# Kernel tuning notes

Measured on AMD Instinct MI355X. Metric: run time of the kernel, lower is better.

Reference implementation:

```python
import jax, jax.numpy as jnp
import numpy as np


def setup_inputs() -> dict:
    key = jax.random.key(0)
    k1, k2, k3 = jax.random.split(key, 3)
    B, S, D, O, C = 4, 1024, 1024, 1024, 8
    x = jax.random.normal(k1, (B, S, D), dtype=jnp.float32)
    category_id = jax.random.randint(k2, (B, S), 0, C, dtype=jnp.int64)
    weight = jax.random.normal(k3, (C, D, O), dtype=jnp.float32)
    bias = jnp.zeros((C, O), dtype=jnp.float32)
    return {"x": x, "category_id": category_id, "weight": weight, "bias": bias}


def reference(x, category_id, weight, bias):
    # Faithful to: out[t] = x[t] @ weight[cid[t]] + bias[cid[t]]
    # Instead of gathering a full [T, D, O] per-token weight tensor (the torch
    # original's bmm formulation), compute x against every category's matrix and
    # select the row for each token's category -- same math, far less memory.
    orig_shape = x.shape
    T = np.prod(orig_shape[:-1])
    x_flat = x.reshape(T, orig_shape[-1])            # [T, D]
    cid = category_id.reshape(T)                      # [T]
    y_all = jnp.einsum('td,cdo->tco', x_flat, weight)  # [T, C, O]
    y = jnp.take_along_axis(y_all, cid[:, None, None], axis=1)[:, 0, :]  # [T, O]
    out = y + bias[cid]                               # [T, O]
    return out.reshape(*orig_shape[:-1], out.shape[-1])
```

## Files before the change

kernel.cpp:

```cpp
#include <hip/hip_runtime.h>


typedef __attribute__((ext_vector_type(8))) short bf16x8;
typedef __attribute__((ext_vector_type(4))) float f32x4;
typedef __attribute__((ext_vector_type(8))) unsigned short ushort8_t;

__device__ __forceinline__ unsigned short f2bf(float f) {
  unsigned u = __float_as_uint(f);
  u += 0x7FFFu + ((u >> 16) & 1u);
  return (unsigned short)(u >> 16);
}

__device__ __forceinline__ void gload_lds16(const unsigned short* g, unsigned short* l) {
  __builtin_amdgcn_global_load_lds(
      (const __attribute__((address_space(1))) unsigned int*)g,
      (__attribute__((address_space(3))) unsigned int*)l, 16, 0, 0);
}

#define MAXC 8

__global__ void k_prep(const float* __restrict__ W, unsigned short* __restrict__ Wt,
                       int Dd, int Oo,
                       const float* __restrict__ x, unsigned short* __restrict__ xb, int nX,
                       const int* __restrict__ cid, int* __restrict__ counts,
                       int* __restrict__ bucket, int T, int C, int tpw) {
  int b   = blockIdx.x;
  int tid = threadIdx.x;

  if (b == 0) {
    __shared__ int cnt[256][MAXC];
    int tpt = (T + 255) / 256;
    int t0  = tid * tpt;
    int t1  = min(t0 + tpt, T);
    for (int c = 0; c < C; ++c) cnt[tid][c] = 0;
    for (int t = t0; t < t1; ++t) cnt[tid][cid[t]]++;
    __syncthreads();
    if (tid < C) {
      int run = 0;
      for (int t = 0; t < 256; ++t) { int v = cnt[t][tid]; cnt[t][tid] = run; run += v; }
      counts[tid] = run;
    }
    __syncthreads();
    for (int t = t0; t < t1; ++t) {
      int c = cid[t];
      int p = cnt[tid][c]++;
      bucket[c * T + p] = t;
    }
    return;
  }

  if (b > tpw) {
    int i = ((b - tpw - 1) * 256 + tid) * 8;
    if (i >= nX) return;
    float4 a0 = *reinterpret_cast<const float4*>(x + i);
    float4 a1 = *reinterpret_cast<const float4*>(x + i + 4);
    ushort8_t o;
    o[0] = f2bf(a0.x); o[1] = f2bf(a0.y); o[2] = f2bf(a0.z); o[3] = f2bf(a0.w);
    o[4] = f2bf(a1.x); o[5] = f2bf(a1.y); o[6] = f2bf(a1.z); o[7] = f2bf(a1.w);
    *reinterpret_cast<ushort8_t*>(xb + i) = o;
    return;
  }

  int bb  = b - 1;
  int tpc = (Dd / 64) * (Oo / 64);
  int c   = bb / tpc;
  int rem = bb % tpc;
  int d0  = (rem / (Oo / 64)) * 64;
  int o0  = (rem % (Oo / 64)) * 64;

  __shared__ float t[64][65];
  const float* Wc = W + (size_t)c * Dd * Oo;
#pragma unroll
  for (int p = 0; p < 4; ++p) {
    int chunk = p * 256 + tid;
    int r  = chunk >> 4;
    int cb = chunk & 15;
    float4 v = *reinterpret_cast<const float4*>(Wc + (size_t)(d0 + r) * Oo + o0 + cb * 4);
    t[r][cb * 4 + 0] = v.x; t[r][cb * 4 + 1] = v.y;
    t[r][cb * 4 + 2] = v.z; t[r][cb * 4 + 3] = v.w;
  }
  __syncthreads();
  unsigned short* Wtc = Wt + (size_t)c * Oo * Dd;
#pragma unroll
  for (int p = 0; p < 2; ++p) {
    int chunk = p * 256 + tid;
    int orow = chunk >> 3;
    int dseg = chunk & 7;
    ushort8_t w;
#pragma unroll
    for (int j = 0; j < 8; ++j) w[j] = f2bf(t[dseg * 8 + j][orow]);
    *reinterpret_cast<ushort8_t*>(Wtc + (size_t)(o0 + orow) * Dd + d0 + dseg * 8) = w;
  }
}

#define BM 128
#define BN 128
#define BK 64
#define TILE_A (BM * BK)
#define TILE_B (BN * BK)

__global__ __launch_bounds__(1024) void k_ggemm(
    const unsigned short* __restrict__ xb, const unsigned short* __restrict__ Wt,
    const float* __restrict__ bias, const int* __restrict__ counts,
    const int* __restrict__ bucket, float* __restrict__ out,
    int T, int Dd, int Oo) {
  int c  = blockIdx.x;
  int Mc = counts[c];
  int m0 = blockIdx.z * BM;
  if (m0 >= Mc) return;
  int n0 = blockIdx.y * BN;

  extern __shared__ __align__(16) unsigned short smem[];
  unsigned short* Al = smem;
  unsigned short* Bl = smem + 3 * TILE_A;

  const int tid  = threadIdx.x;
  const int lane = tid & 63;
  const int wid  = tid >> 6;
  const int wm   = wid >> 2, wn = wid & 3;

  const int* buck = bucket + c * T;
  const unsigned short* Wc = Wt + (size_t)c * Oo * Dd;

  const unsigned short* aSrc;
  const unsigned short* bSrc;
  int sOff;
  {
    int row = wid * 8 + (lane >> 3);
    int seg = (lane & 7) ^ (row & 7);
    int mr  = m0 + row;
    int tok = buck[mr < Mc ? mr : Mc - 1];
    aSrc = xb + (size_t)tok * Dd + seg * 8;
    bSrc = Wc + (size_t)(n0 + row) * Dd + seg * 8;
    sOff = (wid * 8) * BK;
  }

  float bias_r[2];
#pragma unroll
  for (int ni = 0; ni < 2; ++ni)
    bias_r[ni] = bias[c * Oo + n0 + wn * 32 + ni * 16 + (lane & 15)];

  const f32x4 fzero = {0.f, 0.f, 0.f, 0.f};
  f32x4 acc[2][2];
#pragma unroll
  for (int i = 0; i < 2; ++i)
#pragma unroll
    for (int j = 0; j < 2; ++j) acc[i][j] = fzero;

  const int KT = Dd / BK;

#pragma unroll
  for (int t8 = 0; t8 < 2; ++t8) {
    int ko = t8 * BK;
    gload_lds16(aSrc + ko, Al + t8 * TILE_A + sOff);
    gload_lds16(bSrc + ko, Bl + t8 * TILE_B + sOff);
  }

  for (int kt = 0; kt < KT; ++kt) {
    int cur = kt % 3;
    asm volatile("s_waitcnt lgkmcnt(0)" ::: "memory");
    if (kt < KT - 1) {
      asm volatile("s_waitcnt vmcnt(2)" ::: "memory");
    } else {
      asm volatile("s_waitcnt vmcnt(0)" ::: "memory");
    }
    __builtin_amdgcn_sched_barrier(0);
    __builtin_amdgcn_s_barrier();
    __builtin_amdgcn_sched_barrier(0);

    int nb = (cur + 2 >= 3) ? cur - 1 : cur + 2;
    if (kt + 2 < KT) gload_lds16(aSrc + (kt + 2) * BK, Al + nb * TILE_A + sOff);
    {
      bf16x8 af[2], bf[2];
#pragma unroll
      for (int mi = 0; mi < 2; ++mi) {
        int row  = wm * 32 + mi * 16 + (lane & 15);
        int slot = (lane >> 4) ^ (row & 7);
        af[mi] = *reinterpret_cast<const bf16x8*>(&Al[cur * TILE_A + row * BK + slot * 8]);
      }
#pragma unroll
      for (int ni = 0; ni < 2; ++ni) {
        int row  = wn * 32 + ni * 16 + (lane & 15);
        int slot = (lane >> 4) ^ (row & 7);
        bf[ni] = *reinterpret_cast<const bf16x8*>(&Bl[cur * TILE_B + row * BK + slot * 8]);
      }
      __builtin_amdgcn_s_setprio(1);
#pragma unroll
      for (int mi = 0; mi < 2; ++mi)
#pragma unroll
        for (int ni = 0; ni < 2; ++ni)
          acc[mi][ni] = __builtin_amdgcn_mfma_f32_16x16x32_bf16(af[mi], bf[ni], acc[mi][ni], 0, 0, 0);
      __builtin_amdgcn_s_setprio(0);
    }
    __builtin_amdgcn_sched_barrier(0);
    __builtin_amdgcn_s_barrier();
    __builtin_amdgcn_sched_barrier(0);
    if (kt + 2 < KT) gload_lds16(bSrc + (kt + 2) * BK, Bl + nb * TILE_B + sOff);
    {
      bf16x8 af[2], bf[2];
#pragma unroll
      for (int mi = 0; mi < 2; ++mi) {
        int row  = wm * 32 + mi * 16 + (lane & 15);
        int slot = (4 + (lane >> 4)) ^ (row & 7);
        af[mi] = *reinterpret_cast<const bf16x8*>(&Al[cur * TILE_A + row * BK + slot * 8]);
      }
#pragma unroll
      for (int ni = 0; ni < 2; ++ni) {
        int row  = wn * 32 + ni * 16 + (lane & 15);
        int slot = (4 + (lane >> 4)) ^ (row & 7);
        bf[ni] = *reinterpret_cast<const bf16x8*>(&Bl[cur * TILE_B + row * BK + slot * 8]);
      }
      __builtin_amdgcn_s_setprio(1);
#pragma unroll
      for (int mi = 0; mi < 2; ++mi)
#pragma unroll
        for (int ni = 0; ni < 2; ++ni)
          acc[mi][ni] = __builtin_amdgcn_mfma_f32_16x16x32_bf16(af[mi], bf[ni], acc[mi][ni], 0, 0, 0);
      __builtin_amdgcn_s_setprio(0);
    }
  }

#pragma unroll
  for (int mi = 0; mi < 2; ++mi) {
    int rb = m0 + wm * 32 + mi * 16 + (lane >> 4) * 4;
#pragma unroll
    for (int r = 0; r < 4; ++r) {
      int mrow = rb + r;
      if (mrow < Mc) {
        int tok = buck[mrow];
        float* orow = out + (size_t)tok * Oo;
#pragma unroll
        for (int ni = 0; ni < 2; ++ni) {
          int col = n0 + wn * 32 + ni * 16 + (lane & 15);
          orow[col] = acc[mi][ni][r] + bias_r[ni];
        }
      }
    }
  }
}

extern "C" void kernel_launch(void* const* d_in, const int* in_sizes, int n_in,
                              void* d_out, int out_size, void* d_ws, size_t ws_size,
                              hipStream_t stream) {
  const float* x    = (const float*)d_in[0];
  const int*   cid  = (const int*)d_in[1];
  const float* W    = (const float*)d_in[2];
  const float* bias = (const float*)d_in[3];
  float* out = (float*)d_out;

  int T = in_sizes[1];
  int D = in_sizes[0] / T;
  int O = out_size / T;
  int C = in_sizes[3] / O;

  char* ws = (char*)d_ws;
  int* counts = (int*)ws;
  int* bucket = (int*)(ws + 64);
  unsigned short* xb = (unsigned short*)(ws + 64 + (size_t)C * T * 4);
  unsigned short* Wt = xb + (size_t)T * D;

  int tpw  = C * (D / 64) * (O / 64);
  int cvtb = (T * D / 8 + 255) / 256;
  k_prep<<<1 + tpw + cvtb, 256, 0, stream>>>(W, Wt, D, O, x, xb, T * D,
                                             cid, counts, bucket, T, C, tpw);
  size_t ldsBytes = (size_t)3 * (TILE_A + TILE_B) * sizeof(unsigned short);
  k_ggemm<<<dim3(C, O / BN, (T + BM - 1) / BM), 1024, ldsBytes, stream>>>(
      xb, Wt, bias, counts, bucket, out, T, D, O);
}
```

Measured before the change: 48.47 us.

## Double the K tile and switch to a two-stage LDS pipeline

Raises BK from 64 to 128 and replaces the three-buffer, two-half-step prefetch with a simpler double buffer. Each iteration now issues the whole next tile's loads up front, then runs four MFMA sub-steps, with one barrier per iteration instead of two. This halves the number of K iterations and barriers. In exchange, prefetch distance drops to one tile and every iteration waits with vmcnt(0), so load latency may be less hidden. The s_setprio hints are removed and the swizzle widens to 16 slots.

```diff
diff --git a/kernel.cpp b/kernel.cpp
--- a/kernel.cpp
+++ b/kernel.cpp
@@ -95,7 +95,7 @@
 
 #define BM 128
 #define BN 128
-#define BK 64
+#define BK 128
 #define TILE_A (BM * BK)
 #define TILE_B (BN * BK)
 
@@ -112,7 +112,7 @@
 
   extern __shared__ __align__(16) unsigned short smem[];
   unsigned short* Al = smem;
-  unsigned short* Bl = smem + 3 * TILE_A;
+  unsigned short* Bl = smem + 2 * TILE_A;
 
   const int tid  = threadIdx.x;
   const int lane = tid & 63;
@@ -122,17 +122,18 @@
   const int* buck = bucket + c * T;
   const unsigned short* Wc = Wt + (size_t)c * Oo * Dd;
 
-  const unsigned short* aSrc;
-  const unsigned short* bSrc;
-  int sOff;
-  {
-    int row = wid * 8 + (lane >> 3);
-    int seg = (lane & 7) ^ (row & 7);
+  const unsigned short* aSrc[2];
+  const unsigned short* bSrc[2];
+  int sOff[2];
+#pragma unroll
+  for (int i = 0; i < 2; ++i) {
+    int row = wid * 8 + i * 4 + (lane >> 4);
+    int seg = (lane & 15) ^ (row & 15);
     int mr  = m0 + row;
     int tok = buck[mr < Mc ? mr : Mc - 1];
-    aSrc = xb + (size_t)tok * Dd + seg * 8;
-    bSrc = Wc + (size_t)(n0 + row) * Dd + seg * 8;
-    sOff = (wid * 8) * BK;
+    aSrc[i] = xb + (size_t)tok * Dd + seg * 8;
+    bSrc[i] = Wc + (size_t)(n0 + row) * Dd + seg * 8;
+    sOff[i] = (wid * 8 + i * 4) * BK;
   }
 
   float bias_r[2];
@@ -150,73 +151,52 @@
   const int KT = Dd / BK;
 
 #pragma unroll
-  for (int t8 = 0; t8 < 2; ++t8) {
-    int ko = t8 * BK;
-    gload_lds16(aSrc + ko, Al + t8 * TILE_A + sOff);
-    gload_lds16(bSrc + ko, Bl + t8 * TILE_B + sOff);
-  }
+  for (int i = 0; i < 2; ++i) {
+    gload_lds16(aSrc[i], Al + sOff[i]);
+    gload_lds16(bSrc[i], Bl + sOff[i]);
+  }
+  asm volatile("s_waitcnt vmcnt(0)" ::: "memory");
+  __builtin_amdgcn_sched_barrier(0);
+  __builtin_amdgcn_s_barrier();
 
   for (int kt = 0; kt < KT; ++kt) {
-    int cur = kt % 3;
-    asm volatile("s_waitcnt lgkmcnt(0)" ::: "memory");
-    if (kt < KT - 1) {
-      asm volatile("s_waitcnt vmcnt(2)" ::: "memory");
-    } else {
-      asm volatile("s_waitcnt vmcnt(0)" ::: "memory");
-    }
-    __builtin_amdgcn_sched_barrier(0);
-    __builtin_amdgcn_s_barrier();
-    __builtin_amdgcn_sched_barrier(0);
-
-    int nb = (cur + 2 >= 3) ? cur - 1 : cur + 2;
-    if (kt + 2 < KT) gload_lds16(aSrc + (kt + 2) * BK, Al + nb * TILE_A + sOff);
-    {
+    int cur = kt & 1;
+    if (kt + 1 < KT) {
+      int ko = (kt + 1) * BK;
+      int nb = cur ^ 1;
+#pragma unroll
+      for (int i = 0; i < 2; ++i) {
+        gload_lds16(aSrc[i] + ko, Al + nb * TILE_A + sOff[i]);
+        gload_lds16(bSrc[i] + ko, Bl + nb * TILE_B + sOff[i]);
+      }
+    }
+#pragma unroll
+    for (int kk = 0; kk < 4; ++kk) {
       bf16x8 af[2], bf[2];
 #pragma unroll
       for (int mi = 0; mi < 2; ++mi) {
         int row  = wm * 32 + mi * 16 + (lane & 15);
-        int slot = (lane >> 4) ^ (row & 7);
+        int slot = (kk * 4 + (lane >> 4)) ^ (row & 15);
         af[mi] = *reinterpret_cast<const bf16x8*>(&Al[cur * TILE_A + row * BK + slot * 8]);
       }
 #pragma unroll
       for (int ni = 0; ni < 2; ++ni) {
         int row  = wn * 32 + ni * 16 + (lane & 15);
-        int slot = (lane >> 4) ^ (row & 7);
+        int slot = (kk * 4 + (lane >> 4)) ^ (row & 15);
         bf[ni] = *reinterpret_cast<const bf16x8*>(&Bl[cur * TILE_B + row * BK + slot * 8]);
       }
-      __builtin_amdgcn_s_setprio(1);
 #pragma unroll
       for (int mi = 0; mi < 2; ++mi)
 #pragma unroll
         for (int ni = 0; ni < 2; ++ni)
           acc[mi][ni] = __builtin_amdgcn_mfma_f32_16x16x32_bf16(af[mi], bf[ni], acc[mi][ni], 0, 0, 0);
-      __builtin_amdgcn_s_setprio(0);
-    }
-    __builtin_amdgcn_sched_barrier(0);
-    __builtin_amdgcn_s_barrier();
-    __builtin_amdgcn_sched_barrier(0);
-    if (kt + 2 < KT) gload_lds16(bSrc + (kt + 2) * BK, Bl + nb * TILE_B + sOff);
-    {
-      bf16x8 af[2], bf[2];
-#pragma unroll
-      for (int mi = 0; mi < 2; ++mi) {
-        int row  = wm * 32 + mi * 16 + (lane & 15);
-        int slot = (4 + (lane >> 4)) ^ (row & 7);
-        af[mi] = *reinterpret_cast<const bf16x8*>(&Al[cur * TILE_A + row * BK + slot * 8]);
-      }
-#pragma unroll
-      for (int ni = 0; ni < 2; ++ni) {
-        int row  = wn * 32 + ni * 16 + (lane & 15);
-        int slot = (4 + (lane >> 4)) ^ (row & 7);
-        bf[ni] = *reinterpret_cast<const bf16x8*>(&Bl[cur * TILE_B + row * BK + slot * 8]);
-      }
-      __builtin_amdgcn_s_setprio(1);
-#pragma unroll
-      for (int mi = 0; mi < 2; ++mi)
-#pragma unroll
-        for (int ni = 0; ni < 2; ++ni)
-          acc[mi][ni] = __builtin_amdgcn_mfma_f32_16x16x32_bf16(af[mi], bf[ni], acc[mi][ni], 0, 0, 0);
-      __builtin_amdgcn_s_setprio(0);
+    }
+    if (kt + 1 < KT) {
+      asm volatile("s_waitcnt lgkmcnt(0)" ::: "memory");
+      asm volatile("s_waitcnt vmcnt(0)" ::: "memory");
+      __builtin_amdgcn_sched_barrier(0);
+      __builtin_amdgcn_s_barrier();
+      __builtin_amdgcn_sched_barrier(0);
     }
   }
 
@@ -263,7 +243,7 @@
   int cvtb = (T * D / 8 + 255) / 256;
   k_prep<<<1 + tpw + cvtb, 256, 0, stream>>>(W, Wt, D, O, x, xb, T * D,
                                              cid, counts, bucket, T, C, tpw);
-  size_t ldsBytes = (size_t)3 * (TILE_A + TILE_B) * sizeof(unsigned short);
+  size_t ldsBytes = (size_t)2 * (TILE_A + TILE_B) * sizeof(unsigned short);
   k_ggemm<<<dim3(C, O / BN, (T + BM - 1) / BM), 1024, ldsBytes, stream>>>(
       xb, Wt, bias, counts, bucket, out, T, D, O);
 }
```

Result: faster. 47.02 us (-3.0%).
